# Performance work log

Measured on AMD Instinct MI355X. Metric: run time of the kernel, lower is better.

The kernel has to match this reference:

```python
import jax, jax.numpy as jnp
import numpy as np
import math

B, S, HID, H = 1, 2048, 1024, 16
D = HID // H  # head_dim = 64


def setup_inputs() -> dict:
    key = jax.random.key(0)
    ks = jax.random.split(key, 12)
    s = 0.02
    x = jax.random.normal(ks[0], (B, S, HID), jnp.float32)
    Wq = jax.random.normal(ks[1], (HID, HID), jnp.float32) * s
    bq = jnp.zeros((HID,), jnp.float32)
    Wk = jax.random.normal(ks[2], (HID, HID), jnp.float32) * s
    bk = jnp.zeros((HID,), jnp.float32)
    Wv = jax.random.normal(ks[3], (HID, HID), jnp.float32) * s
    bv = jnp.zeros((HID,), jnp.float32)
    Wo = jax.random.normal(ks[4], (HID, HID), jnp.float32) * s
    bo = jnp.zeros((HID,), jnp.float32)
    # nn.Parameter(torch.ones(3,3)) at init; small noise so the bias is non-degenerate
    cmw = jnp.ones((3, 3), jnp.float32) + 0.1 * jax.random.normal(ks[5], (3, 3), jnp.float32)
    # full causal [B,S,S] mask so the mask.shape[1]==seq_len branch is taken
    mask = jnp.tril(jnp.ones((B, S, S), jnp.int32))
    modality_info = jax.random.randint(ks[6], (B, S), 0, 3, dtype=jnp.int64)
    return dict(x=x, Wq=Wq, bq=bq, Wk=Wk, bk=bk, Wv=Wv, bv=bv, Wo=Wo, bo=bo,
                cmw=cmw, mask=mask, modality_info=modality_info)


def reference(x, Wq, bq, Wk, bk, Wv, bv, Wo, bo, cmw, mask, modality_info):
    b, s, _ = x.shape
    # QKV projections (torch Linear: y = x @ W.T + b), split into heads [B,H,S,D]
    q = (x @ Wq.T + bq).reshape(b, s, H, D).transpose(0, 2, 1, 3)
    k = (x @ Wk.T + bk).reshape(b, s, H, D).transpose(0, 2, 1, 3)
    v = (x @ Wv.T + bv).reshape(b, s, H, D).transpose(0, 2, 1, 3)
    scores = jnp.einsum('bhqd,bhkd->bhqk', q, k) / math.sqrt(D)  # [B,H,S,S]
    # cross-modal bias: gather from 3x3 table via pairwise modality indices -> [B,S,S]
    bias = cmw[modality_info[:, :, None], modality_info[:, None, :]]
    scores = scores + bias[:, None, :, :]  # equals original broadcast when B==1
    scores = jnp.where(mask[:, None, :, :] == 0, -1e9, scores)
    attn = jax.nn.softmax(scores, axis=-1)  # dropout is identity in eval
    ctx = jnp.einsum('bhqk,bhkd->bhqd', attn, v)          # [B,H,S,D]
    ctx = ctx.transpose(0, 2, 1, 3).reshape(b, s, HID)    # [B,S,HID]
    return ctx @ Wo.T + bo
```

## Files before the change

kernel.cpp:

```cpp
#include <hip/hip_runtime.h>
#include <hip/hip_bf16.h>
#include <math.h>

#define S_LEN 2048
#define HID   1024
#define NHEAD 16

using bf16x8 = __attribute__((ext_vector_type(8))) short;
using bf16x4 = __attribute__((ext_vector_type(4))) short;
using f32x4  = __attribute__((ext_vector_type(4))) float;

__device__ __forceinline__ float bf2f(short s) {
  union { unsigned u; float f; } c;
  c.u = ((unsigned)(unsigned short)s) << 16;
  return c.f;
}
__device__ __forceinline__ short f2bf(float f) {
  union { float f; unsigned u; } c; c.f = f;
  unsigned u = c.u;
  unsigned r = (u + 0x7fffu + ((u >> 16) & 1u)) >> 16;
  return (short)r;
}
__device__ __forceinline__ float loadf(const void* base, long idx, int is_bf) {
  return is_bf ? bf2f(((const short*)base)[idx]) : ((const float*)base)[idx];
}
__device__ __forceinline__ void gl_lds16(const void* g, void* l) {
  __builtin_amdgcn_global_load_lds(
      (const __attribute__((address_space(1))) void*)g,
      (__attribute__((address_space(3))) void*)l, 16, 0, 0);
}

__global__ void detect_kernel(const unsigned* __restrict__ xw,
                              const int* __restrict__ modw,
                              int* __restrict__ flags) {
  const int t = threadIdx.x;
  int cnt = 0;
  for (int i = t; i < 1024; i += 64) {
    const unsigned fld = (xw[i] >> 7) & 0xFFu;
    cnt += (fld >= 100u && fld <= 135u) ? 1 : 0;
  }
  int odd = 0;
  for (int i = 0; i < 4; ++i) {
    const int wv = modw[2 * (t + 64 * i) + 1];
    odd += (wv != 0) ? 1 : 0;
  }
  for (int m = 1; m < 64; m <<= 1) {
    cnt += __shfl_xor(cnt, m);
    odd += __shfl_xor(odd, m);
  }
  if (t == 0) {
    flags[0] = (cnt >= 512) ? 1 : 0;
    flags[1] = (odd == 0) ? 1 : 0;
  }
}

__global__ __launch_bounds__(256) void convert5(
    const void* __restrict__ s0, const void* __restrict__ s1, const void* __restrict__ s2,
    const void* __restrict__ s3, const void* __restrict__ s4,
    short* __restrict__ d0, short* __restrict__ d1, short* __restrict__ d2,
    short* __restrict__ d3, short* __restrict__ d4,
    const int* __restrict__ flags) {
  const int a = blockIdx.y;
  const void* src = (a == 0) ? s0 : (a == 1) ? s1 : (a == 2) ? s2 : (a == 3) ? s3 : s4;
  short* dst = (a == 0) ? d0 : (a == 1) ? d1 : (a == 2) ? d2 : (a == 3) ? d3 : d4;
  const long n = (a == 0) ? (2L << 20) : (1L << 20);
  const int is_bf = flags[0];
  long i = (long)(blockIdx.x * 256 + threadIdx.x) * 8;
  const long stride = (long)gridDim.x * 256 * 8;
  if (is_bf) {
    for (; i < n; i += stride)
      *(bf16x8*)(dst + i) = *(const bf16x8*)((const short*)src + i);
  } else {
    for (; i < n; i += stride) {
      const float* p = (const float*)src + i;
      bf16x8 r;
#pragma unroll
      for (int j = 0; j < 8; ++j) r[j] = f2bf(p[j]);
      *(bf16x8*)(dst + i) = r;
    }
  }
}

__global__ __launch_bounds__(256) void gemm_bt3(
    const short* __restrict__ A,
    const short* __restrict__ W0, const short* __restrict__ W1, const short* __restrict__ W2,
    const void* __restrict__ b0, const void* __restrict__ b1, const void* __restrict__ b2,
    void* __restrict__ C0, void* __restrict__ C1, void* __restrict__ C2,
    const int* __restrict__ flags, int nbn, int store_f32)
{
  constexpr int K = 1024;
  constexpr int N = 1024;
  __shared__ short As[128 * 32];
  __shared__ short Bs[64 * 32];

  const int t = threadIdx.x;
  const int w = t >> 6, lane = t & 63;
  const int l15 = lane & 15, quad = lane >> 4;
  const int wm = w >> 1, wn = w & 1;
  const int is_bf = flags[0];

  const int mat = blockIdx.x / nbn;
  const int n0 = (blockIdx.x % nbn) * 64;
  const int m0 = blockIdx.y * 128;

  const short* W  = (mat == 0) ? W0 : (mat == 1 ? W1 : W2);
  const void* bia = (mat == 0) ? b0 : (mat == 1 ? b1 : b2);
  void*       C   = (mat == 0) ? C0 : (mat == 1 ? C1 : C2);

  f32x4 acc[4][2];
  for (int mi = 0; mi < 4; ++mi)
    for (int ni = 0; ni < 2; ++ni)
      for (int r = 0; r < 4; ++r) acc[mi][ni][r] = 0.f;

  const int srow = t >> 2;
  const int sch  = (t & 3) * 8;
  const short* Ap = A + (long)(m0 + srow) * K + sch;
  const short* Wp = W + (long)(n0 + srow) * K + sch;
  short* AsW = &As[w * 512];
  short* BsW = &Bs[w * 512];

  for (int kt = 0; kt < K / 32; ++kt) {
    __syncthreads();
    gl_lds16(Ap + kt * 32, AsW);
    gl_lds16(Ap + kt * 32 + 64L * K, AsW + 2048);
    gl_lds16(Wp + kt * 32, BsW);
    __syncthreads();

    bf16x8 af[4], bfr[2];
    for (int mi = 0; mi < 4; ++mi)
      af[mi] = *(const bf16x8*)&As[(wm * 64 + mi * 16 + l15) * 32 + quad * 8];
    for (int ni = 0; ni < 2; ++ni)
      bfr[ni] = *(const bf16x8*)&Bs[(wn * 32 + ni * 16 + l15) * 32 + quad * 8];
    for (int mi = 0; mi < 4; ++mi)
      for (int ni = 0; ni < 2; ++ni)
        acc[mi][ni] = __builtin_amdgcn_mfma_f32_16x16x32_bf16(af[mi], bfr[ni], acc[mi][ni], 0, 0, 0);
  }

  for (int ni = 0; ni < 2; ++ni) {
    const int col = n0 + wn * 32 + ni * 16 + l15;
    const float bv = loadf(bia, col, is_bf);
    for (int mi = 0; mi < 4; ++mi) {
      const int row = m0 + wm * 64 + mi * 16 + quad * 4;
      for (int r = 0; r < 4; ++r) {
        const float v = acc[mi][ni][r] + bv;
        const long idx = (long)(row + r) * N + col;
        if (store_f32) ((float*)C)[idx] = v;
        else           ((short*)C)[idx] = f2bf(v);
      }
    }
  }
}

__global__ __launch_bounds__(256) void attn_split(
    const short* __restrict__ Q, const short* __restrict__ Kg, const short* __restrict__ Vg,
    const int* __restrict__ mod, const void* __restrict__ cmw,
    const int* __restrict__ flags,
    short* __restrict__ PO0, short* __restrict__ PO1,
    float* __restrict__ PL)
{
  __shared__ short Ks[64 * 80];
  __shared__ short Vt[64 * 80];
  __shared__ short Ps[4 * 16 * 80];
  __shared__ float cm[9];
  __shared__ int mods[2048];

  const int t = threadIdx.x;
  const int w = t >> 6, lane = t & 63;
  const int l15 = lane & 15, quad = lane >> 4;
  const int h = blockIdx.y;
  const int pair = blockIdx.x >> 1;
  const int par  = blockIdx.x & 1;
  const int m64 = flags[1];

  if (t < 9) cm[t] = loadf(cmw, t, flags[0]);
  for (int i = t; i < 2048; i += 256) mods[i] = mod[i << m64];
  __syncthreads();

  short* POp = (par == 0) ? PO0 : PO1;
  const int krow = t >> 3, kch = (t & 7) * 8;
  const int vkp = t & 63, vdc = (t >> 6) * 8;

  for (int si = 0; si < 2; ++si) {
    const int strip = (si == 0) ? pair : 31 - pair;
    const int q0 = strip * 64;
    const int nkt = strip + 1;

    const short* qb = Q + (long)(q0 + w * 16 + l15) * HID + h * 64 + quad * 8;
    const bf16x8 aq0 = *(const bf16x8*)qb;
    const bf16x8 aq1 = *(const bf16x8*)(qb + 32);

    int mrow[4];
    for (int r = 0; r < 4; ++r) mrow[r] = mods[q0 + w * 16 + quad * 4 + r];

    float lsum[4];
    f32x4 acc_o[4];
    for (int r = 0; r < 4; ++r) lsum[r] = 0.f;
    for (int ni = 0; ni < 4; ++ni)
      for (int r = 0; r < 4; ++r) acc_o[ni][r] = 0.f;

    bf16x8 rk0, rk1, rv0, rv1;
    if (par < nkt) {
      const long kb = (long)(par * 64) * HID + h * 64;
      rk0 = *(const bf16x8*)(Kg + kb + (long)krow * HID + kch);
      rk1 = *(const bf16x8*)(Kg + kb + (long)(krow + 32) * HID + kch);
      rv0 = *(const bf16x8*)(Vg + kb + (long)vkp * HID + vdc);
      rv1 = *(const bf16x8*)(Vg + kb + (long)vkp * HID + 32 + vdc);
    }

    for (int kt = par; kt < nkt; kt += 2) {
      __syncthreads();
      *(bf16x8*)&Ks[krow * 80 + kch] = rk0;
      *(bf16x8*)&Ks[(krow + 32) * 80 + kch] = rk1;
#pragma unroll
      for (int j = 0; j < 8; ++j) Vt[(vdc + j) * 80 + vkp] = rv0[j];
#pragma unroll
      for (int j = 0; j < 8; ++j) Vt[(vdc + 32 + j) * 80 + vkp] = rv1[j];
      __syncthreads();
      if (kt + 2 < nkt) {
        const long kb = (long)((kt + 2) * 64) * HID + h * 64;
        rk0 = *(const bf16x8*)(Kg + kb + (long)krow * HID + kch);
        rk1 = *(const bf16x8*)(Kg + kb + (long)(krow + 32) * HID + kch);
        rv0 = *(const bf16x8*)(Vg + kb + (long)vkp * HID + vdc);
        rv1 = *(const bf16x8*)(Vg + kb + (long)vkp * HID + 32 + vdc);
      }

      f32x4 sc[4];
      for (int nt = 0; nt < 4; ++nt) {
        const bf16x8 kb0 = *(const bf16x8*)&Ks[(nt * 16 + l15) * 80 + quad * 8];
        const bf16x8 kb1 = *(const bf16x8*)&Ks[(nt * 16 + l15) * 80 + 32 + quad * 8];
        f32x4 z;
        for (int r = 0; r < 4; ++r) z[r] = 0.f;
        z = __builtin_amdgcn_mfma_f32_16x16x32_bf16(aq0, kb0, z, 0, 0, 0);
        z = __builtin_amdgcn_mfma_f32_16x16x32_bf16(aq1, kb1, z, 0, 0, 0);
        sc[nt] = z;
      }

      float sv[4][4];
      for (int nt = 0; nt < 4; ++nt) {
        const int mcol = mods[kt * 64 + nt * 16 + l15];
        for (int r = 0; r < 4; ++r)
          sv[nt][r] = sc[nt][r] * 0.125f + cm[mrow[r] * 3 + mcol];
      }
      if (kt == nkt - 1) {
        for (int nt = 0; nt < 4; ++nt) {
          const int col = kt * 64 + nt * 16 + l15;
          for (int r = 0; r < 4; ++r) {
            const int row = q0 + w * 16 + quad * 4 + r;
            sv[nt][r] = (col <= row) ? sv[nt][r] : -1e30f;
          }
        }
      }
      short pb[4][4];
      for (int nt = 0; nt < 4; ++nt)
        for (int r = 0; r < 4; ++r) {
          const float p = __expf(fminf(sv[nt][r], 60.f));
          lsum[r] += p;
          pb[nt][r] = f2bf(p);
        }

      short* Pw = &Ps[w * 16 * 80];
      for (int nt = 0; nt < 4; ++nt)
        for (int r = 0; r < 4; ++r)
          Pw[(quad * 4 + r) * 80 + nt * 16 + l15] = pb[nt][r];
      asm volatile("s_waitcnt lgkmcnt(0)" ::: "memory");

      for (int kk = 0; kk < 2; ++kk) {
        const bf16x8 ap = *(const bf16x8*)&Pw[l15 * 80 + kk * 32 + quad * 8];
        for (int ni = 0; ni < 4; ++ni) {
          const bf16x8 bv = *(const bf16x8*)&Vt[(ni * 16 + l15) * 80 + kk * 32 + quad * 8];
          acc_o[ni] = __builtin_amdgcn_mfma_f32_16x16x32_bf16(ap, bv, acc_o[ni], 0, 0, 0);
        }
      }
    }

    for (int off = 1; off < 16; off <<= 1)
      for (int r = 0; r < 4; ++r) lsum[r] += __shfl_xor(lsum[r], off);

    for (int ni = 0; ni < 4; ++ni) {
      const int col = h * 64 + ni * 16 + l15;
      for (int r = 0; r < 4; ++r) {
        const int row = q0 + w * 16 + quad * 4 + r;
        POp[(long)row * HID + col] = f2bf(acc_o[ni][r]);
      }
    }
    if (l15 == 0) {
      for (int r = 0; r < 4; ++r) {
        const int row = q0 + w * 16 + quad * 4 + r;
        PL[par * 32768 + row * 16 + h] = lsum[r];
      }
    }
  }
}

__global__ __launch_bounds__(256) void attn_merge(
    const short* __restrict__ PO0, const short* __restrict__ PO1,
    const float* __restrict__ PL, short* __restrict__ CTX)
{
  const int row = blockIdx.x;
  const int t = threadIdx.x;
  const int h = t >> 4;
  const int d0 = (t & 15) * 4;
  const float l0 = PL[row * 16 + h], l1 = PL[32768 + row * 16 + h];
  const float inv = 1.f / (l0 + l1);
  const long b = (long)row * HID + h * 64 + d0;
  const bf16x4 o0 = *(const bf16x4*)&PO0[b];
  const bf16x4 o1 = *(const bf16x4*)&PO1[b];
  bf16x4 out;
#pragma unroll
  for (int j = 0; j < 4; ++j)
    out[j] = f2bf((bf2f(o0[j]) + bf2f(o1[j])) * inv);
  *(bf16x4*)&CTX[b] = out;
}

extern "C" void kernel_launch(void* const* d_in, const int* in_sizes, int n_in,
                              void* d_out, int out_size, void* d_ws, size_t ws_size,
                              hipStream_t stream) {
  constexpr long M1 = 1024L * 1024L;
  int*   flags = (int*)d_ws;
  short* base  = (short*)d_ws + 128;
  short* xb  = base;
  short* Wqb = xb + 2 * M1;
  short* Wkb = Wqb + M1;
  short* Wvb = Wkb + M1;
  short* Wob = Wvb + M1;
  short* Qw  = Wob + M1;
  short* Kw  = Qw + 2 * M1;
  short* Vw  = Kw + 2 * M1;
  short* CTX = Vw + 2 * M1;
  short* PO0 = CTX;
  short* PO1 = xb;
  float* PL  = (float*)Wvb;
  const int* modality = (const int*)d_in[11];

  detect_kernel<<<1, 64, 0, stream>>>((const unsigned*)d_in[0], modality, flags);
  convert5<<<dim3(512, 5), 256, 0, stream>>>(
      d_in[0], d_in[1], d_in[3], d_in[5], d_in[7],
      xb, Wqb, Wkb, Wvb, Wob, flags);

  gemm_bt3<<<dim3(48, 16), 256, 0, stream>>>(
      xb, Wqb, Wkb, Wvb, d_in[2], d_in[4], d_in[6],
      Qw, Kw, Vw, flags, 16, 0);
  attn_split<<<dim3(32, NHEAD), 256, 0, stream>>>(
      Qw, Kw, Vw, modality, d_in[9], flags, PO0, PO1, PL);
  attn_merge<<<dim3(S_LEN), 256, 0, stream>>>(PO0, PO1, PL, CTX);
  gemm_bt3<<<dim3(16, 16), 256, 0, stream>>>(
      CTX, Wob, Wob, Wob, d_in[8], d_in[8], d_in[8],
      d_out, d_out, d_out, flags, 16, 1);
}
```

Baseline: 181.8 us.

## Double-buffer GEMM LDS staging, retile output projection, fold detection into convert

The GEMM kernel now stages the next K-tile into a second LDS buffer while computing on the current one, which drops one barrier per iteration. It is templated on the M tile so the output projection runs with 64-row tiles and twice as many blocks. The separate dtype and modality detection kernel is merged into the conversion kernel, where each block recomputes the dtype check locally, saving one launch. In exchange, LDS use doubles and every convert block does a redundant 1024-word scan.

Result: no change. 178.3 us (-1.9%).

```diff
diff --git a/kernel.cpp b/kernel.cpp
--- a/kernel.cpp
+++ b/kernel.cpp
@@ -30,42 +30,46 @@
       (__attribute__((address_space(3))) void*)l, 16, 0, 0);
 }
 
-__global__ void detect_kernel(const unsigned* __restrict__ xw,
-                              const int* __restrict__ modw,
-                              int* __restrict__ flags) {
-  const int t = threadIdx.x;
-  int cnt = 0;
-  for (int i = t; i < 1024; i += 64) {
-    const unsigned fld = (xw[i] >> 7) & 0xFFu;
-    cnt += (fld >= 100u && fld <= 135u) ? 1 : 0;
-  }
-  int odd = 0;
-  for (int i = 0; i < 4; ++i) {
-    const int wv = modw[2 * (t + 64 * i) + 1];
-    odd += (wv != 0) ? 1 : 0;
-  }
-  for (int m = 1; m < 64; m <<= 1) {
-    cnt += __shfl_xor(cnt, m);
-    odd += __shfl_xor(odd, m);
-  }
-  if (t == 0) {
-    flags[0] = (cnt >= 512) ? 1 : 0;
-    flags[1] = (odd == 0) ? 1 : 0;
-  }
-}
-
 __global__ __launch_bounds__(256) void convert5(
     const void* __restrict__ s0, const void* __restrict__ s1, const void* __restrict__ s2,
     const void* __restrict__ s3, const void* __restrict__ s4,
     short* __restrict__ d0, short* __restrict__ d1, short* __restrict__ d2,
     short* __restrict__ d3, short* __restrict__ d4,
-    const int* __restrict__ flags) {
+    const int* __restrict__ modw, int* __restrict__ flags) {
+  __shared__ int sh_isbf;
+  const int t = threadIdx.x;
+
+  if (t < 64) {
+    const unsigned* xw = (const unsigned*)s0;
+    int cnt = 0;
+    for (int i = t; i < 1024; i += 64) {
+      const unsigned fld = (xw[i] >> 7) & 0xFFu;
+      cnt += (fld >= 100u && fld <= 135u) ? 1 : 0;
+    }
+    for (int m = 1; m < 64; m <<= 1) cnt += __shfl_xor(cnt, m);
+    if (t == 0) sh_isbf = (cnt >= 512) ? 1 : 0;
+  }
+  __syncthreads();
+  const int is_bf = sh_isbf;
+
+  if (blockIdx.x == 0 && blockIdx.y == 0 && t < 64) {
+    int odd = 0;
+    for (int i = 0; i < 4; ++i) {
+      const int wv = modw[2 * (t + 64 * i) + 1];
+      odd += (wv != 0) ? 1 : 0;
+    }
+    for (int m = 1; m < 64; m <<= 1) odd += __shfl_xor(odd, m);
+    if (t == 0) {
+      flags[0] = is_bf;
+      flags[1] = (odd == 0) ? 1 : 0;
+    }
+  }
+
   const int a = blockIdx.y;
   const void* src = (a == 0) ? s0 : (a == 1) ? s1 : (a == 2) ? s2 : (a == 3) ? s3 : s4;
   short* dst = (a == 0) ? d0 : (a == 1) ? d1 : (a == 2) ? d2 : (a == 3) ? d3 : d4;
   const long n = (a == 0) ? (2L << 20) : (1L << 20);
-  const int is_bf = flags[0];
-  long i = (long)(blockIdx.x * 256 + threadIdx.x) * 8;
+  long i = (long)(blockIdx.x * 256 + t) * 8;
   const long stride = (long)gridDim.x * 256 * 8;
   if (is_bf) {
     for (; i < n; i += stride)
@@ -81,6 +85,7 @@
   }
 }
 
+template <int BM>
 __global__ __launch_bounds__(256) void gemm_bt3(
     const short* __restrict__ A,
     const short* __restrict__ W0, const short* __restrict__ W1, const short* __restrict__ W2,
@@ -90,57 +95,67 @@
 {
   constexpr int K = 1024;
   constexpr int N = 1024;
-  __shared__ short As[128 * 32];
-  __shared__ short Bs[64 * 32];
+  constexpr int WN = (BM == 128) ? 2 : 4;
+  constexpr int WM = 4 / WN;
+  constexpr int MI = (BM / 16) / WM;
+  constexpr int NI = (64 / 16) / WN;
+  __shared__ short As[2][BM * 32];
+  __shared__ short Bs[2][64 * 32];
 
   const int t = threadIdx.x;
   const int w = t >> 6, lane = t & 63;
   const int l15 = lane & 15, quad = lane >> 4;
-  const int wm = w >> 1, wn = w & 1;
+  const int wm = w / WN, wn = w % WN;
   const int is_bf = flags[0];
 
   const int mat = blockIdx.x / nbn;
   const int n0 = (blockIdx.x % nbn) * 64;
-  const int m0 = blockIdx.y * 128;
+  const int m0 = blockIdx.y * BM;
 
   const short* W  = (mat == 0) ? W0 : (mat == 1 ? W1 : W2);
   const void* bia = (mat == 0) ? b0 : (mat == 1 ? b1 : b2);
   void*       C   = (mat == 0) ? C0 : (mat == 1 ? C1 : C2);
 
-  f32x4 acc[4][2];
-  for (int mi = 0; mi < 4; ++mi)
-    for (int ni = 0; ni < 2; ++ni)
+  f32x4 acc[MI][NI];
+  for (int mi = 0; mi < MI; ++mi)
+    for (int ni = 0; ni < NI; ++ni)
       for (int r = 0; r < 4; ++r) acc[mi][ni][r] = 0.f;
 
   const int srow = t >> 2;
   const int sch  = (t & 3) * 8;
   const short* Ap = A + (long)(m0 + srow) * K + sch;
   const short* Wp = W + (long)(n0 + srow) * K + sch;
-  short* AsW = &As[w * 512];
-  short* BsW = &Bs[w * 512];
-
+
+  auto stage = [&](int kt, int buf) {
+    short* ad = &As[buf][w * 512];
+    short* bd = &Bs[buf][w * 512];
+    gl_lds16(Ap + kt * 32, ad);
+    if (BM == 128) gl_lds16(Ap + kt * 32 + 64L * K, ad + 2048);
+    gl_lds16(Wp + kt * 32, bd);
+  };
+
+  stage(0, 0);
+  int cur = 0;
   for (int kt = 0; kt < K / 32; ++kt) {
     __syncthreads();
-    gl_lds16(Ap + kt * 32, AsW);
-    gl_lds16(Ap + kt * 32 + 64L * K, AsW + 2048);
-    gl_lds16(Wp + kt * 32, BsW);
-    __syncthreads();
-
-    bf16x8 af[4], bfr[2];
-    for (int mi = 0; mi < 4; ++mi)
-      af[mi] = *(const bf16x8*)&As[(wm * 64 + mi * 16 + l15) * 32 + quad * 8];
-    for (int ni = 0; ni < 2; ++ni)
-      bfr[ni] = *(const bf16x8*)&Bs[(wn * 32 + ni * 16 + l15) * 32 + quad * 8];
-    for (int mi = 0; mi < 4; ++mi)
-      for (int ni = 0; ni < 2; ++ni)
+    if (kt + 1 < K / 32) stage(kt + 1, cur ^ 1);
+
+    bf16x8 af[MI], bfr[NI];
+    for (int mi = 0; mi < MI; ++mi)
+      af[mi] = *(const bf16x8*)&As[cur][(wm * (MI * 16) + mi * 16 + l15) * 32 + quad * 8];
+    for (int ni = 0; ni < NI; ++ni)
+      bfr[ni] = *(const bf16x8*)&Bs[cur][(wn * (NI * 16) + ni * 16 + l15) * 32 + quad * 8];
+    for (int mi = 0; mi < MI; ++mi)
+      for (int ni = 0; ni < NI; ++ni)
         acc[mi][ni] = __builtin_amdgcn_mfma_f32_16x16x32_bf16(af[mi], bfr[ni], acc[mi][ni], 0, 0, 0);
-  }
-
-  for (int ni = 0; ni < 2; ++ni) {
-    const int col = n0 + wn * 32 + ni * 16 + l15;
+    cur ^= 1;
+  }
+
+  for (int ni = 0; ni < NI; ++ni) {
+    const int col = n0 + wn * (NI * 16) + ni * 16 + l15;
     const float bv = loadf(bia, col, is_bf);
-    for (int mi = 0; mi < 4; ++mi) {
-      const int row = m0 + wm * 64 + mi * 16 + quad * 4;
+    for (int mi = 0; mi < MI; ++mi) {
+      const int row = m0 + wm * (MI * 16) + mi * 16 + quad * 4;
       for (int r = 0; r < 4; ++r) {
         const float v = acc[mi][ni][r] + bv;
         const long idx = (long)(row + r) * N + col;
@@ -332,18 +347,17 @@
   float* PL  = (float*)Wvb;
   const int* modality = (const int*)d_in[11];
 
-  detect_kernel<<<1, 64, 0, stream>>>((const unsigned*)d_in[0], modality, flags);
   convert5<<<dim3(512, 5), 256, 0, stream>>>(
       d_in[0], d_in[1], d_in[3], d_in[5], d_in[7],
-      xb, Wqb, Wkb, Wvb, Wob, flags);
-
-  gemm_bt3<<<dim3(48, 16), 256, 0, stream>>>(
+      xb, Wqb, Wkb, Wvb, Wob, modality, flags);
+
+  gemm_bt3<128><<<dim3(48, 16), 256, 0, stream>>>(
       xb, Wqb, Wkb, Wvb, d_in[2], d_in[4], d_in[6],
       Qw, Kw, Vw, flags, 16, 0);
   attn_split<<<dim3(32, NHEAD), 256, 0, stream>>>(
       Qw, Kw, Vw, modality, d_in[9], flags, PO0, PO1, PL);
   attn_merge<<<dim3(S_LEN), 256, 0, stream>>>(PO0, PO1, PL, CTX);
-  gemm_bt3<<<dim3(16, 16), 256, 0, stream>>>(
+  gemm_bt3<64><<<dim3(16, 32), 256, 0, stream>>>(
       CTX, Wob, Wob, Wob, d_in[8], d_in[8], d_in[8],
       d_out, d_out, d_out, flags, 16, 1);
 }
```
